# Kernel tuning notes

Measured on AMD Instinct MI355X. Metric: run time of the kernel, lower is better.

## Reference

```python
import jax, jax.numpy as jnp
import numpy as np

K = 3
STRIDE = 1
PADDING = 1


def unfold(x, k, stride, padding):
    # torch.nn.functional.unfold: patches ordered (C, kh, kw), positions row-major
    N, C, H, W = x.shape
    xp = jnp.pad(x, ((0, 0), (0, 0), (padding, padding), (padding, padding)))
    H_out = (H - k + 2 * padding) // stride + 1
    W_out = (W - k + 2 * padding) // stride + 1
    patches = jnp.stack(
        [xp[:, :, i:i + stride * H_out:stride, j:j + stride * W_out:stride]
         for i in range(k) for j in range(k)],
        axis=2,
    )  # (N, C, k*k, H_out, W_out)
    return patches.reshape(N, C * k * k, H_out * W_out), H_out, W_out


def setup_inputs() -> dict:
    key = jax.random.key(0)
    k1, k2 = jax.random.split(key)
    x = jax.random.normal(k1, (16, 64, 14, 14), dtype=jnp.float32)
    W = jax.random.normal(k2, (64, 64, 3, 3), dtype=jnp.float32)
    return {"x": x, "W": W}


def reference(x, W):
    F_out = W.shape[0]
    X_col, H_out, W_out = unfold(x, K, STRIDE, PADDING)  # (N, D, P)
    W_col = W.reshape(F_out, -1)                          # (F, D)
    # AdderNet: out[n,f,p] = -sum_d |W[f,d] - X[n,d,p]|
    out = -jnp.sum(jnp.abs(W_col[None, :, :, None] - X_col[:, None, :, :]), axis=2)  # (N, F, P)
    return out.reshape(x.shape[0], F_out, H_out, W_out)
```

## Files before the change

kernel.cpp:

```cpp
#include <hip/hip_runtime.h>


#define N_ 16
#define C_ 64
#define F_ 64
#define P_ 196

__global__ __launch_bounds__(256, 4) void adder2d_kernel(
    const float* __restrict__ x, const float* __restrict__ w,
    float* __restrict__ out)
{
    __shared__ __align__(16) float xs[16 * 48];
    __shared__ float part[4][64 * 15];

    const int tid = threadIdx.x;
    const int row = blockIdx.x;
    const int n   = blockIdx.y;
    const int cs  = blockIdx.z;
    const int f   = tid & 63;
    const int wid = tid >> 6;
    const int cbase = cs * 16 + wid * 4;

    #pragma unroll
    for (int i = 0; i < 3; ++i) {
        const int idx = tid + 256 * i;
        const int c   = idx / 48;
        const int rem = idx - c * 48;
        const int r   = rem >> 4;
        const int col = rem & 15;
        const int ir  = row + r - 1;
        float v = 0.f;
        if (col >= 1 && col <= 14 && ir >= 0 && ir <= 13)
            v = x[(n * C_ + cs * 16 + c) * P_ + ir * 14 + (col - 1)];
        xs[idx] = v;
    }

    float Wr[36];
    {
        const float4* wp = (const float4*)(w + f * (C_ * 9) + cbase * 9);
        #pragma unroll
        for (int i = 0; i < 9; ++i) {
            float4 t = wp[i];
            Wr[4 * i + 0] = t.x; Wr[4 * i + 1] = t.y;
            Wr[4 * i + 2] = t.z; Wr[4 * i + 3] = t.w;
        }
    }

    float acc[14];
    #pragma unroll
    for (int p = 0; p < 14; ++p) acc[p] = 0.f;

    __syncthreads();

    const float* xb = xs + (wid * 4) * 48;
    #pragma unroll
    for (int cl = 0; cl < 4; ++cl) {
        #pragma unroll
        for (int kh = 0; kh < 3; ++kh) {
            const float4* rp = (const float4*)(xb + cl * 48 + kh * 16);
            float4 q0 = rp[0], q1 = rp[1], q2 = rp[2], q3 = rp[3];
            float xr[16] = {q0.x, q0.y, q0.z, q0.w,  q1.x, q1.y, q1.z, q1.w,
                            q2.x, q2.y, q2.z, q2.w,  q3.x, q3.y, q3.z, q3.w};
            #pragma unroll
            for (int kw = 0; kw < 3; ++kw) {
                const float wv = Wr[cl * 9 + kh * 3 + kw];
                #pragma unroll
                for (int p = 0; p < 14; ++p)
                    acc[p] += fabsf(wv - xr[p + kw]);
            }
        }
    }

    #pragma unroll
    for (int p = 0; p < 14; ++p) part[wid][f * 15 + p] = acc[p];
    __syncthreads();

    for (int o = tid; o < 896; o += 256) {
        const int ff = o / 14;
        const int px = o - ff * 14;
        const int a  = ff * 15 + px;
        float s = part[0][a] + part[1][a] + part[2][a] + part[3][a];
        atomicAdd(&out[(n * F_ + ff) * P_ + row * 14 + px], -s);
    }
}

extern "C" void kernel_launch(void* const* d_in, const int* in_sizes, int n_in,
                              void* d_out, int out_size, void* d_ws, size_t ws_size,
                              hipStream_t stream) {
    const float* x = (const float*)d_in[0];
    const float* w = (const float*)d_in[1];
    float* out = (float*)d_out;
    hipMemsetAsync(out, 0, (size_t)out_size * sizeof(float), stream);
    dim3 grid(14, N_, 4);
    adder2d_kernel<<<grid, 256, 0, stream>>>(x, w, out);
}
```

Measured before the change: 69.27 us.

## Split work by output columns instead of channels, dropping atomics and memset

Each block now covers all 64 input channels for half of an output row (7 columns) instead of a quarter of the channels for the full row. The partial sums are written with plain stores, so the separate memset launch and the global atomicAdds go away. The cost is that each block loads more x data into LDS and each thread reloads weights in four chunks, and the grid has half as many blocks (448 instead of 896).

```diff
diff --git a/kernel.cpp b/kernel.cpp
--- a/kernel.cpp
+++ b/kernel.cpp
@@ -6,81 +6,85 @@
 #define F_ 64
 #define P_ 196
 
-__global__ __launch_bounds__(256, 4) void adder2d_kernel(
+__global__ __launch_bounds__(256, 2) void adder2d_kernel(
     const float* __restrict__ x, const float* __restrict__ w,
     float* __restrict__ out)
 {
-    __shared__ __align__(16) float xs[16 * 48];
-    __shared__ float part[4][64 * 15];
+    __shared__ __align__(16) float xs[64 * 36];
+    __shared__ float part[4][64 * 9];
 
     const int tid = threadIdx.x;
     const int row = blockIdx.x;
     const int n   = blockIdx.y;
-    const int cs  = blockIdx.z;
+    const int z   = blockIdx.z;
     const int f   = tid & 63;
     const int wid = tid >> 6;
-    const int cbase = cs * 16 + wid * 4;
 
     #pragma unroll
-    for (int i = 0; i < 3; ++i) {
+    for (int i = 0; i < 9; ++i) {
         const int idx = tid + 256 * i;
-        const int c   = idx / 48;
-        const int rem = idx - c * 48;
-        const int r   = rem >> 4;
-        const int col = rem & 15;
+        const int c   = idx / 36;
+        const int rem = idx - c * 36;
+        const int r   = rem / 12;
+        const int j   = rem - r * 12;
         const int ir  = row + r - 1;
+        const int ic  = z * 7 + j - 1;
         float v = 0.f;
-        if (col >= 1 && col <= 14 && ir >= 0 && ir <= 13)
-            v = x[(n * C_ + cs * 16 + c) * P_ + ir * 14 + (col - 1)];
+        if (ic >= 0 && ic <= 13 && ir >= 0 && ir <= 13)
+            v = x[(n * C_ + c) * P_ + ir * 14 + ic];
         xs[idx] = v;
     }
 
-    float Wr[36];
-    {
-        const float4* wp = (const float4*)(w + f * (C_ * 9) + cbase * 9);
-        #pragma unroll
-        for (int i = 0; i < 9; ++i) {
-            float4 t = wp[i];
-            Wr[4 * i + 0] = t.x; Wr[4 * i + 1] = t.y;
-            Wr[4 * i + 2] = t.z; Wr[4 * i + 3] = t.w;
-        }
-    }
-
-    float acc[14];
+    float acc[7];
     #pragma unroll
-    for (int p = 0; p < 14; ++p) acc[p] = 0.f;
+    for (int p = 0; p < 7; ++p) acc[p] = 0.f;
 
     __syncthreads();
 
-    const float* xb = xs + (wid * 4) * 48;
     #pragma unroll
-    for (int cl = 0; cl < 4; ++cl) {
+    for (int q = 0; q < 4; ++q) {
+        const int cb = wid * 16 + q * 4;
+        float Wr[36];
+        {
+            const float4* wp = (const float4*)(w + f * (C_ * 9) + cb * 9);
+            #pragma unroll
+            for (int i = 0; i < 9; ++i) {
+                float4 t = wp[i];
+                Wr[4 * i + 0] = t.x; Wr[4 * i + 1] = t.y;
+                Wr[4 * i + 2] = t.z; Wr[4 * i + 3] = t.w;
+            }
+        }
+        const float* xb = xs + cb * 36;
         #pragma unroll
-        for (int kh = 0; kh < 3; ++kh) {
-            const float4* rp = (const float4*)(xb + cl * 48 + kh * 16);
-            float4 q0 = rp[0], q1 = rp[1], q2 = rp[2], q3 = rp[3];
-            float xr[16] = {q0.x, q0.y, q0.z, q0.w,  q1.x, q1.y, q1.z, q1.w,
-                            q2.x, q2.y, q2.z, q2.w,  q3.x, q3.y, q3.z, q3.w};
+        for (int cl = 0; cl < 4; ++cl) {
             #pragma unroll
-            for (int kw = 0; kw < 3; ++kw) {
-                const float wv = Wr[cl * 9 + kh * 3 + kw];
+            for (int kh = 0; kh < 3; ++kh) {
+                const float4* rp = (const float4*)(xb + cl * 36 + kh * 12);
+                float4 a0 = rp[0], a1 = rp[1], a2 = rp[2];
+                float xr[12] = {a0.x, a0.y, a0.z, a0.w,
+                                a1.x, a1.y, a1.z, a1.w,
+                                a2.x, a2.y, a2.z, a2.w};
                 #pragma unroll
-                for (int p = 0; p < 14; ++p)
-                    acc[p] += fabsf(wv - xr[p + kw]);
+                for (int kw = 0; kw < 3; ++kw) {
+                    const float wv = Wr[cl * 9 + kh * 3 + kw];
+                    #pragma unroll
+                    for (int p = 0; p < 7; ++p)
+                        acc[p] += fabsf(wv - xr[p + kw]);
+                }
             }
         }
     }
 
     #pragma unroll
-    for (int p = 0; p < 14; ++p) part[wid][f * 15 + p] = acc[p];
+    for (int p = 0; p < 7; ++p) part[wid][f * 9 + p] = acc[p];
     __syncthreads();
 
-    for (int o = tid; o < 896; o += 256) {
-        const int ff = o / 14;
-        const int px = o - ff * 14;
-        const int a  = ff * 15 + px;
+    for (int o = tid; o < 448; o += 256) {
+        const int ff = o / 7;
+        const int px = o - ff * 7;
+        const int a  = ff * 9 + px;
         float s = part[0][a] + part[1][a] + part[2][a] + part[3][a];
-        atomicAdd(&out[(n * F_ + ff) * P_ + row * 14 + px], -s);
+        out[(n * F_ + ff) * P_ + row * 14 + z * 7 + px] = -s;
     }
 }
 
@@ -90,7 +94,6 @@
     const float* x = (const float*)d_in[0];
     const float* w = (const float*)d_in[1];
     float* out = (float*)d_out;
-    hipMemsetAsync(out, 0, (size_t)out_size * sizeof(float), stream);
-    dim3 grid(14, N_, 4);
+    dim3 grid(14, N_, 2);
     adder2d_kernel<<<grid, 256, 0, stream>>>(x, w, out);
 }
```

Result: no change. 69.36 us (+0.1%).
